# Kernel optimization log

Measured on AMD Instinct MI355X. Metric: run time of the kernel, lower is better.

## Reference

```python
import jax, jax.numpy as jnp
import numpy as np
import math

NUM_HEADS = 16
D_KV = 64
D_MODEL = 1024
NUM_BUCKETS = 32
MAX_DISTANCE = 128
SEQ = 2048
BATCH = 2


def _relative_position_bucket(relative_position):
    # bidirectional T5 bucketing
    num_buckets = NUM_BUCKETS // 2  # 16
    buckets = (relative_position > 0).astype(jnp.int32) * num_buckets
    rp = jnp.abs(relative_position)
    max_exact = num_buckets // 2  # 8
    is_small = rp < max_exact
    rp_safe = jnp.maximum(rp, 1)  # avoid log(0); masked by is_small anyway
    rp_large = max_exact + (
        jnp.log(rp_safe.astype(jnp.float32) / max_exact)
        / math.log(MAX_DISTANCE / max_exact)
        * (num_buckets - max_exact)
    ).astype(jnp.int32)
    rp_large = jnp.minimum(rp_large, num_buckets - 1)
    return buckets + jnp.where(is_small, rp, rp_large)


def _position_bias(rel_bias_table, q_len, k_len):
    ctx = jnp.arange(q_len)[:, None]
    mem = jnp.arange(k_len)[None, :]
    buckets = _relative_position_bucket(mem - ctx)  # (q,k)
    vals = rel_bias_table[buckets]  # (q,k,h)
    return jnp.transpose(vals, (2, 0, 1))[None]  # (1,h,q,k)


def setup_inputs() -> dict:
    key = jax.random.key(0)
    ks = jax.random.split(key, 6)
    s = 1.0 / math.sqrt(D_MODEL)
    return {
        "hidden_states": jax.random.normal(ks[0], (BATCH, SEQ, D_MODEL), jnp.float32),
        "Wq": jax.random.normal(ks[1], (D_MODEL, NUM_HEADS * D_KV), jnp.float32) * s,
        "Wk": jax.random.normal(ks[2], (D_MODEL, NUM_HEADS * D_KV), jnp.float32) * s,
        "Wv": jax.random.normal(ks[3], (D_MODEL, NUM_HEADS * D_KV), jnp.float32) * s,
        "Wo": jax.random.normal(ks[4], (NUM_HEADS * D_KV, D_MODEL), jnp.float32) * s,
        "rel_bias_table": jax.random.normal(ks[5], (NUM_BUCKETS, NUM_HEADS), jnp.float32),
    }


def reference(hidden_states, Wq, Wk, Wv, Wo, rel_bias_table):
    b, s, _ = hidden_states.shape
    q = (hidden_states @ Wq).reshape(b, s, NUM_HEADS, D_KV).transpose(0, 2, 1, 3)
    k = (hidden_states @ Wk).reshape(b, s, NUM_HEADS, D_KV).transpose(0, 2, 1, 3)
    v = (hidden_states @ Wv).reshape(b, s, NUM_HEADS, D_KV).transpose(0, 2, 1, 3)
    # T5: NO query scaling, additive relative-position bias
    scores = jnp.einsum("bhqd,bhkd->bhqk", q, k) + _position_bias(rel_bias_table, s, s)
    attn = jax.nn.softmax(scores, axis=-1)  # dropout is identity in eval
    out = jnp.einsum("bhqk,bhkd->bhqd", attn, v)
    out = out.transpose(0, 2, 1, 3).reshape(b, s, NUM_HEADS * D_KV)
    return out @ Wo
```

## Files before the change

### kernel.cpp

```cpp
#include <hip/hip_runtime.h>
#include <hip/hip_bf16.h>
#include <math.h>

#define NUM_HEADS 16
#define D_KV 64
#define D_MODEL 1024
#define SEQ 2048
#define BATCH 2
#define LOG2E 1.4426950408889634f

using bf16x8 = __attribute__((ext_vector_type(8))) short;
using bf16x4 = __attribute__((ext_vector_type(4))) short;
using f32x4  = __attribute__((ext_vector_type(4))) float;

__device__ inline unsigned short f2bf(float f) {
  union { float f; unsigned int i; } v; v.f = f;
  unsigned int u = v.i;
  return (unsigned short)((u + 0x7FFFu + ((u >> 16) & 1u)) >> 16);
}
__device__ inline unsigned short f2bf_fast(float f) {
  union { float f; unsigned int i; } v; v.f = f;
  return (unsigned short)((v.i + 0x8000u) >> 16);
}

#if __has_builtin(__builtin_amdgcn_exp2f)
#define EXP2(x) __builtin_amdgcn_exp2f(x)
#else
#define EXP2(x) __expf((x) * 0.6931471805599453f)
#endif

__device__ inline unsigned int pk_bf16(float a, float b) {
#if __has_builtin(__builtin_amdgcn_cvt_pk_bf16_f32)
  auto v = __builtin_amdgcn_cvt_pk_bf16_f32(a, b);
  unsigned int u; __builtin_memcpy(&u, &v, 4);
  return u;
#else
  return ((unsigned int)f2bf_fast(b) << 16) | f2bf_fast(a);
#endif
}

__device__ inline void gld_lds16(const unsigned short* g, unsigned short* l) {
  __builtin_amdgcn_global_load_lds(
      (const __attribute__((address_space(1))) unsigned int*)g,
      (__attribute__((address_space(3))) unsigned int*)l, 16, 0, 0);
}

__global__ __launch_bounds__(256) void prep_kernel(const float* __restrict__ X,
                                                   const float* __restrict__ W0,
                                                   const float* __restrict__ W1,
                                                   const float* __restrict__ W2,
                                                   const float* __restrict__ W3,
                                                   const float* __restrict__ tbl,
                                                   unsigned short* __restrict__ xbf,
                                                   unsigned short* __restrict__ wt,
                                                   float* __restrict__ biasF) {
  __shared__ __align__(16) unsigned short T[64][72];
  int bid = blockIdx.x;
  int t = threadIdx.x;
  if (bid < 2048) {
    int i = (bid * 256 + t) * 8;
    __align__(16) unsigned short tmp[8];
#pragma unroll
    for (int e = 0; e < 8; e++) tmp[e] = f2bf(X[i + e]);
    *(uint4*)&xbf[i] = *(uint4*)tmp;
  } else if (bid < 3072) {
    int rem = bid - 2048;
    int z = rem >> 8, tid = rem & 255;
    const float* in = (z == 0) ? W0 : (z == 1) ? W1 : (z == 2) ? W2 : W3;
    unsigned short* o = wt + (long)z * 1048576;
    int r0 = (tid & 15) * 64, c0 = (tid >> 4) * 64;
#pragma unroll
    for (int i = 0; i < 2; i++) {
      int c = t + 256 * i; int r = c >> 3, k8 = (c & 7) * 8;
      const float* src = &in[(long)(r0 + r) * 1024 + c0 + k8];
      __align__(16) unsigned short tmp[8];
#pragma unroll
      for (int e = 0; e < 8; e++) tmp[e] = f2bf(src[e]);
      *(uint4*)&T[r][k8] = *(uint4*)tmp;
    }
    __syncthreads();
#pragma unroll
    for (int i = 0; i < 2; i++) {
      int c = t + 256 * i; int r = c >> 3, k8 = (c & 7) * 8;
      __align__(16) unsigned short tmp[8];
#pragma unroll
      for (int e = 0; e < 8; e++) tmp[e] = T[k8 + e][r];
      *(uint4*)&o[(long)(c0 + r) * 1024 + r0 + k8] = *(uint4*)tmp;
    }
  } else {
#pragma unroll
    for (int ii = 0; ii < 16; ii++) {
      int idx = t + 256 * ii;
      if (idx >= 4095) break;
      int rel = idx - 2047;
      int bucket = (rel > 0) ? 16 : 0;
      int rp = rel < 0 ? -rel : rel;
      int add;
      if (rp < 8) add = rp;
      else {
        int rl = 8 + (int)(logf((float)rp * 0.125f) / logf(16.0f) * 8.0f);
        add = rl < 15 ? rl : 15;
      }
      bucket += add;
#pragma unroll
      for (int h = 0; h < 16; h++) biasF[h * 4096 + idx] = tbl[bucket * 16 + h] * LOG2E;
    }
  }
}

__global__ __launch_bounds__(256) void transpose_b2b(const unsigned short* __restrict__ in,
                                                     unsigned short* __restrict__ out,
                                                     int in_stride, int out_stride,
                                                     long in_bstride, long out_bstride) {
  __shared__ __align__(16) unsigned short T[64][72];
  in  += blockIdx.z * in_bstride;
  out += blockIdx.z * out_bstride;
  int r0 = blockIdx.x * 64, c0 = blockIdx.y * 64;
  int t = threadIdx.x;
#pragma unroll
  for (int i = 0; i < 2; i++) {
    int c = t + 256 * i; int r = c >> 3, k8 = (c & 7) * 8;
    *(uint4*)&T[r][k8] = *(const uint4*)&in[(long)(r0 + r) * in_stride + c0 + k8];
  }
  __syncthreads();
#pragma unroll
  for (int i = 0; i < 2; i++) {
    int c = t + 256 * i; int r = c >> 3, k8 = (c & 7) * 8;
    __align__(16) unsigned short tmp[8];
#pragma unroll
    for (int e = 0; e < 8; e++) tmp[e] = T[k8 + e][r];
    *(uint4*)&out[(long)(c0 + r) * out_stride + r0 + k8] = *(uint4*)tmp;
  }
}

__global__ __launch_bounds__(256) void gemm_kernel(const unsigned short* __restrict__ X,
                                                   const unsigned short* __restrict__ Wt,
                                                   unsigned short* __restrict__ out_b,
                                                   float* __restrict__ out_f, int mode) {
  __shared__ __align__(16) unsigned short As[128 * 32];
  __shared__ __align__(16) unsigned short Bs[128 * 32];
  const int K = 1024;
  int m0 = blockIdx.x * 128;
  int n0 = blockIdx.y * 128;
  const unsigned short* W = Wt + (long)blockIdx.z * 1048576;
  unsigned short* outq = (mode == 0) ? out_b + (long)blockIdx.z * 4194304 : nullptr;
  float scale = (mode == 0 && blockIdx.z == 0) ? LOG2E : 1.0f;
  int t = threadIdx.x;
  int w = t >> 6, l = t & 63;
  int wr = (w >> 1) * 64, wc = (w & 1) * 64;
  int lr = l & 15, lq = l >> 4;
  f32x4 acc[4][4];
#pragma unroll
  for (int i = 0; i < 4; i++)
#pragma unroll
    for (int j = 0; j < 4; j++) acc[i][j] = (f32x4){0.f, 0.f, 0.f, 0.f};

  for (int k0 = 0; k0 < K; k0 += 32) {
#pragma unroll
    for (int i = 0; i < 2; i++) {
      int c = t + 256 * i;
      int r = c >> 2, kc = (c & 3) * 8;
      gld_lds16(&X[(long)(m0 + r) * K + k0 + kc], &As[c * 8]);
      gld_lds16(&W[(long)(n0 + r) * K + k0 + kc], &Bs[c * 8]);
    }
    __syncthreads();
    bf16x8 a[4], b[4];
#pragma unroll
    for (int mi = 0; mi < 4; mi++) a[mi] = *(const bf16x8*)&As[(wr + mi * 16 + lr) * 32 + lq * 8];
#pragma unroll
    for (int ni = 0; ni < 4; ni++) b[ni] = *(const bf16x8*)&Bs[(wc + ni * 16 + lr) * 32 + lq * 8];
#pragma unroll
    for (int mi = 0; mi < 4; mi++)
#pragma unroll
      for (int ni = 0; ni < 4; ni++)
        acc[mi][ni] = __builtin_amdgcn_mfma_f32_16x16x32_bf16(a[mi], b[ni], acc[mi][ni], 0, 0, 0);
    __syncthreads();
  }
#pragma unroll
  for (int mi = 0; mi < 4; mi++)
#pragma unroll
    for (int ni = 0; ni < 4; ni++)
#pragma unroll
      for (int r = 0; r < 4; r++) {
        int m = m0 + wr + mi * 16 + lq * 4 + r;
        int n = n0 + wc + ni * 16 + lr;
        float vf = acc[mi][ni][r] * scale;
        if (mode == 0) {
          int b_ = m >> 11, s = m & 2047, h = n >> 6, d = n & 63;
          outq[(((long)(b_ * NUM_HEADS + h) * SEQ) + s) * 64 + d] = f2bf(vf);
        } else {
          out_f[(long)m * 1024 + n] = vf;
        }
      }
}

__global__ __launch_bounds__(256, 2) void attn_kernel(const unsigned short* __restrict__ Q,
                                                      const unsigned short* __restrict__ Km,
                                                      const unsigned short* __restrict__ Vt,
                                                      const float* __restrict__ biasF,
                                                      unsigned short* __restrict__ O) {
  __shared__ __align__(16) unsigned short Ks[64 * 72];
  __shared__ __align__(16) unsigned short Vs[64 * 72];
  __shared__ __align__(16) float biasRf[2][2176];
  int q0 = blockIdx.x * 128;
  int bh = blockIdx.y;
  int b_ = bh >> 4, h = bh & 15;
  const unsigned short* Qb = Q  + (long)bh * SEQ * 64;
  const unsigned short* Kb = Km + (long)bh * SEQ * 64;
  const unsigned short* Vb = Vt + (long)bh * 64 * SEQ;
  const float* btabF = biasF + h * 4096;
  int t = threadIdx.x;
  int w = t >> 6, l = t & 63;
  int lr = l & 15, lq = l >> 4;
  int qw = w * 32;

  int gbase = 1920 - q0;
  for (int i = t; i < 2176; i += 256) {
    int g0 = gbase + i;     if (g0 > 4094) g0 = 4094;
    int g1 = gbase + i + 1; if (g1 > 4094) g1 = 4094;
    biasRf[0][i] = btabF[g0];
    biasRf[1][i] = btabF[g1];
  }

  bf16x8 aq[2][2];
#pragma unroll
  for (int qt = 0; qt < 2; qt++)
#pragma unroll
    for (int ks = 0; ks < 2; ks++)
      aq[qt][ks] = *(const bf16x8*)&Qb[(long)(q0 + qw + qt * 16 + lr) * 64 + ks * 32 + lq * 8];

  int c0 = t, c1 = t + 256;
  int r0s = c0 >> 3, f0 = (c0 & 7) * 8;
  int r1s = c1 >> 3, f1 = (c1 & 7) * 8;

  uint4 kca = *(const uint4*)&Kb[(long)r0s * 64 + f0];
  uint4 kcb = *(const uint4*)&Kb[(long)r1s * 64 + f1];
  uint4 vca = *(const uint4*)&Vb[(long)r0s * SEQ + f0];
  uint4 vcb = *(const uint4*)&Vb[(long)r1s * SEQ + f1];
  *(uint4*)&Ks[r0s * 72 + f0] = kca;
  *(uint4*)&Ks[r1s * 72 + f1] = kcb;
  *(uint4*)&Vs[r0s * 72 + f0] = vca;
  *(uint4*)&Vs[r1s * 72 + f1] = vcb;

  f32x4 accO[4][2];
  f32x4 accL[2];
#pragma unroll
  for (int qt = 0; qt < 2; qt++) {
    accL[qt] = (f32x4){0.f, 0.f, 0.f, 0.f};
#pragma unroll
    for (int dt = 0; dt < 4; dt++) accO[dt][qt] = (f32x4){0.f, 0.f, 0.f, 0.f};
  }

  bf16x4 ones4;
#pragma unroll
  for (int e = 0; e < 4; e++) ones4[e] = (short)0x3F80;

  int vb = 127 + lq * 4 - qw - lr;
  int bj2 = vb & 1;
  const float* brow = biasRf[bj2];
  int pbc = vb - bj2 - 16;

  for (int k0 = 0; k0 < SEQ; k0 += 64) {
    __syncthreads();
    bool more = (k0 + 64) < SEQ;

    float2 bbl[5][2];
    int pb = pbc + k0;
#pragma unroll
    for (int m = 0; m < 5; m++) {
      bbl[m][0] = *(const float2*)&brow[pb + 16 * m];
      bbl[m][1] = *(const float2*)&brow[pb + 16 * m + 2];
    }

    bf16x8 bk[4][2];
#pragma unroll
    for (int kt = 0; kt < 4; kt++)
#pragma unroll
      for (int ks = 0; ks < 2; ks++)
        bk[kt][ks] = *(const bf16x8*)&Ks[(kt * 16 + lr) * 72 + ks * 32 + lq * 8];

    if (more) {
      const unsigned short* Kn = Kb + (long)(k0 + 64) * 64;
      const unsigned short* Vn = Vb + (k0 + 64);
      kca = *(const uint4*)&Kn[(long)r0s * 64 + f0];
      kcb = *(const uint4*)&Kn[(long)r1s * 64 + f1];
      vca = *(const uint4*)&Vn[(long)r0s * SEQ + f0];
      vcb = *(const uint4*)&Vn[(long)r1s * SEQ + f1];
    }

    f32x4 sacc[4][2];
#pragma unroll
    for (int kt = 0; kt < 4; kt++)
#pragma unroll
      for (int qt = 0; qt < 2; qt++) sacc[kt][qt] = (f32x4){0.f, 0.f, 0.f, 0.f};
#pragma unroll
    for (int ks = 0; ks < 2; ks++)
#pragma unroll
      for (int kt = 0; kt < 4; kt++)
#pragma unroll
        for (int qt = 0; qt < 2; qt++)
          sacc[kt][qt] = __builtin_amdgcn_mfma_f32_16x16x32_bf16(bk[kt][ks], aq[qt][ks], sacc[kt][qt], 0, 0, 0);

    bf16x4 pk[4][2];
#pragma unroll
    for (int kt = 0; kt < 4; kt++)
#pragma unroll
      for (int qt = 0; qt < 2; qt++) {
        int blk = kt - qt + 1;
        float p0 = EXP2(sacc[kt][qt][0] + bbl[blk][0].x);
        float p1 = EXP2(sacc[kt][qt][1] + bbl[blk][0].y);
        float p2 = EXP2(sacc[kt][qt][2] + bbl[blk][1].x);
        float p3 = EXP2(sacc[kt][qt][3] + bbl[blk][1].y);
        unsigned int uu[2] = { pk_bf16(p0, p1), pk_bf16(p2, p3) };
        bf16x4 pv; __builtin_memcpy(&pv, uu, 8);
        pk[kt][qt] = pv;
      }

#pragma unroll
    for (int kt = 0; kt < 4; kt++) {
      bf16x4 va[4];
#pragma unroll
      for (int dt = 0; dt < 4; dt++)
        va[dt] = *(const bf16x4*)&Vs[(dt * 16 + lr) * 72 + kt * 16 + lq * 4];
#pragma unroll
      for (int qt = 0; qt < 2; qt++) {
#pragma unroll
        for (int dt = 0; dt < 4; dt++)
          accO[dt][qt] = __builtin_amdgcn_mfma_f32_16x16x16bf16_1k(va[dt], pk[kt][qt], accO[dt][qt], 0, 0, 0);
        accL[qt] = __builtin_amdgcn_mfma_f32_16x16x16bf16_1k(ones4, pk[kt][qt], accL[qt], 0, 0, 0);
      }
    }

    __syncthreads();
    if (more) {
      *(uint4*)&Ks[r0s * 72 + f0] = kca;
      *(uint4*)&Ks[r1s * 72 + f1] = kcb;
      *(uint4*)&Vs[r0s * 72 + f0] = vca;
      *(uint4*)&Vs[r1s * 72 + f1] = vcb;
    }
  }

#pragma unroll
  for (int qt = 0; qt < 2; qt++) {
    float rl = 1.0f / accL[qt][0];
    int q = q0 + qw + qt * 16 + lr;
#pragma unroll
    for (int dt = 0; dt < 4; dt++) {
      unsigned int s0 = ((unsigned int)f2bf(accO[dt][qt][1] * rl) << 16) | f2bf(accO[dt][qt][0] * rl);
      unsigned int s1 = ((unsigned int)f2bf(accO[dt][qt][3] * rl) << 16) | f2bf(accO[dt][qt][2] * rl);
      *(uint2*)&O[((long)(b_ * SEQ + q)) * 1024 + h * 64 + dt * 16 + lq * 4] = (uint2){s0, s1};
    }
  }
}

extern "C" void kernel_launch(void* const* d_in, const int* in_sizes, int n_in,
                              void* d_out, int out_size, void* d_ws, size_t ws_size,
                              hipStream_t stream) {
  const float* X   = (const float*)d_in[0];
  const float* Wq  = (const float*)d_in[1];
  const float* Wk  = (const float*)d_in[2];
  const float* Wv  = (const float*)d_in[3];
  const float* Wo  = (const float*)d_in[4];
  const float* tbl = (const float*)d_in[5];

  unsigned short* wt    = (unsigned short*)d_ws;
  unsigned short* xbf   = wt + 4 * 1048576;
  unsigned short* q_ws  = xbf + 4194304;
  unsigned short* k_ws  = q_ws + 4194304;
  unsigned short* v_ws  = k_ws + 4194304;
  unsigned short* vt_ws = v_ws + 4194304;
  unsigned short* o_ws  = vt_ws + 4194304;
  float* biasF = (float*)(o_ws + 4194304);

  prep_kernel<<<3073, 256, 0, stream>>>(X, Wq, Wk, Wv, Wo, tbl, xbf, wt, biasF);
  gemm_kernel<<<dim3(32, 8, 3), 256, 0, stream>>>(xbf, wt, q_ws, nullptr, 0);
  transpose_b2b<<<dim3(32, 1, 32), 256, 0, stream>>>(v_ws, vt_ws, 64, 2048, 131072L, 131072L);
  attn_kernel<<<dim3(16, 32), 256, 0, stream>>>(q_ws, k_ws, vt_ws, biasF, o_ws);
  gemm_kernel<<<dim3(32, 8, 1), 256, 0, stream>>>(o_ws, wt + 3 * 1048576, nullptr, (float*)d_out, 1);
}
```

Measured before the change: 216.1 us.

## Fuse V transpose into QKV GEMM epilogue and split attention KV across wave groups

The QKV GEMM now writes V directly in transposed layout, which removes the separate transpose kernel launch and its extra global round trip. The attention kernel moves to 512 threads. Two wave groups each process alternate 64-key blocks for the same 128 queries, and their partial O and row-sum accumulators are merged through shared memory at the end. This doubles the waves available per query tile to hide latency. In exchange it adds a reduction step, uses more LDS, and drops the double bias-row buffer in favour of scalar bias loads.

```diff
diff --git a/kernel.cpp b/kernel.cpp
--- a/kernel.cpp
+++ b/kernel.cpp
@@ -108,34 +108,10 @@
   }
 }
 
-__global__ __launch_bounds__(256) void transpose_b2b(const unsigned short* __restrict__ in,
-                                                     unsigned short* __restrict__ out,
-                                                     int in_stride, int out_stride,
-                                                     long in_bstride, long out_bstride) {
-  __shared__ __align__(16) unsigned short T[64][72];
-  in  += blockIdx.z * in_bstride;
-  out += blockIdx.z * out_bstride;
-  int r0 = blockIdx.x * 64, c0 = blockIdx.y * 64;
-  int t = threadIdx.x;
-#pragma unroll
-  for (int i = 0; i < 2; i++) {
-    int c = t + 256 * i; int r = c >> 3, k8 = (c & 7) * 8;
-    *(uint4*)&T[r][k8] = *(const uint4*)&in[(long)(r0 + r) * in_stride + c0 + k8];
-  }
-  __syncthreads();
-#pragma unroll
-  for (int i = 0; i < 2; i++) {
-    int c = t + 256 * i; int r = c >> 3, k8 = (c & 7) * 8;
-    __align__(16) unsigned short tmp[8];
-#pragma unroll
-    for (int e = 0; e < 8; e++) tmp[e] = T[k8 + e][r];
-    *(uint4*)&out[(long)(c0 + r) * out_stride + r0 + k8] = *(uint4*)tmp;
-  }
-}
-
 __global__ __launch_bounds__(256) void gemm_kernel(const unsigned short* __restrict__ X,
                                                    const unsigned short* __restrict__ Wt,
                                                    unsigned short* __restrict__ out_b,
+                                                   unsigned short* __restrict__ out_vt,
                                                    float* __restrict__ out_f, int mode) {
   __shared__ __align__(16) unsigned short As[128 * 32];
   __shared__ __align__(16) unsigned short Bs[128 * 32];
@@ -176,32 +152,47 @@
         acc[mi][ni] = __builtin_amdgcn_mfma_f32_16x16x32_bf16(a[mi], b[ni], acc[mi][ni], 0, 0, 0);
     __syncthreads();
   }
-#pragma unroll
-  for (int mi = 0; mi < 4; mi++)
-#pragma unroll
-    for (int ni = 0; ni < 4; ni++)
-#pragma unroll
-      for (int r = 0; r < 4; r++) {
-        int m = m0 + wr + mi * 16 + lq * 4 + r;
+
+  if (mode == 0 && blockIdx.z == 2) {
+#pragma unroll
+    for (int mi = 0; mi < 4; mi++)
+#pragma unroll
+      for (int ni = 0; ni < 4; ni++) {
         int n = n0 + wc + ni * 16 + lr;
-        float vf = acc[mi][ni][r] * scale;
-        if (mode == 0) {
-          int b_ = m >> 11, s = m & 2047, h = n >> 6, d = n & 63;
-          outq[(((long)(b_ * NUM_HEADS + h) * SEQ) + s) * 64 + d] = f2bf(vf);
-        } else {
-          out_f[(long)m * 1024 + n] = vf;
+        int h = n >> 6, d = n & 63;
+        int mbase = m0 + wr + mi * 16 + lq * 4;
+        int b2 = mbase >> 11, s = mbase & 2047;
+        unsigned int s0 = ((unsigned int)f2bf(acc[mi][ni][1]) << 16) | f2bf(acc[mi][ni][0]);
+        unsigned int s1 = ((unsigned int)f2bf(acc[mi][ni][3]) << 16) | f2bf(acc[mi][ni][2]);
+        *(uint2*)&out_vt[(((long)(b2 * 16 + h) * 64 + d) << 11) + s] = (uint2){s0, s1};
+      }
+  } else {
+#pragma unroll
+    for (int mi = 0; mi < 4; mi++)
+#pragma unroll
+      for (int ni = 0; ni < 4; ni++)
+#pragma unroll
+        for (int r = 0; r < 4; r++) {
+          int m = m0 + wr + mi * 16 + lq * 4 + r;
+          int n = n0 + wc + ni * 16 + lr;
+          float vf = acc[mi][ni][r] * scale;
+          if (mode == 0) {
+            int b2 = m >> 11, s = m & 2047, h = n >> 6, d = n & 63;
+            outq[(((long)(b2 * NUM_HEADS + h) * SEQ) + s) * 64 + d] = f2bf(vf);
+          } else {
+            out_f[(long)m * 1024 + n] = vf;
+          }
         }
-      }
-}
-
-__global__ __launch_bounds__(256, 2) void attn_kernel(const unsigned short* __restrict__ Q,
-                                                      const unsigned short* __restrict__ Km,
-                                                      const unsigned short* __restrict__ Vt,
-                                                      const float* __restrict__ biasF,
-                                                      unsigned short* __restrict__ O) {
-  __shared__ __align__(16) unsigned short Ks[64 * 72];
-  __shared__ __align__(16) unsigned short Vs[64 * 72];
-  __shared__ __align__(16) float biasRf[2][2176];
+  }
+}
+
+__global__ __launch_bounds__(512) void attn_kernel(const unsigned short* __restrict__ Q,
+                                                   const unsigned short* __restrict__ Km,
+                                                   const unsigned short* __restrict__ Vt,
+                                                   const float* __restrict__ biasF,
+                                                   unsigned short* __restrict__ O) {
+  __shared__ __align__(16) unsigned short KV[4][4608];
+  __shared__ float biasS[2176];
   int q0 = blockIdx.x * 128;
   int bh = blockIdx.y;
   int b_ = bh >> 4, h = bh & 15;
@@ -211,15 +202,14 @@
   const float* btabF = biasF + h * 4096;
   int t = threadIdx.x;
   int w = t >> 6, l = t & 63;
+  int g = w >> 2, wg = w & 3;
   int lr = l & 15, lq = l >> 4;
-  int qw = w * 32;
+  int qw = wg * 32;
 
   int gbase = 1920 - q0;
-  for (int i = t; i < 2176; i += 256) {
-    int g0 = gbase + i;     if (g0 > 4094) g0 = 4094;
-    int g1 = gbase + i + 1; if (g1 > 4094) g1 = 4094;
-    biasRf[0][i] = btabF[g0];
-    biasRf[1][i] = btabF[g1];
+  for (int i = t; i < 2176; i += 512) {
+    int gi = gbase + i; if (gi > 4094) gi = 4094;
+    biasS[i] = btabF[gi];
   }
 
   bf16x8 aq[2][2];
@@ -229,18 +219,16 @@
     for (int ks = 0; ks < 2; ks++)
       aq[qt][ks] = *(const bf16x8*)&Qb[(long)(q0 + qw + qt * 16 + lr) * 64 + ks * 32 + lq * 8];
 
-  int c0 = t, c1 = t + 256;
-  int r0s = c0 >> 3, f0 = (c0 & 7) * 8;
-  int r1s = c1 >> 3, f1 = (c1 & 7) * 8;
-
-  uint4 kca = *(const uint4*)&Kb[(long)r0s * 64 + f0];
-  uint4 kcb = *(const uint4*)&Kb[(long)r1s * 64 + f1];
-  uint4 vca = *(const uint4*)&Vb[(long)r0s * SEQ + f0];
-  uint4 vcb = *(const uint4*)&Vb[(long)r1s * SEQ + f1];
-  *(uint4*)&Ks[r0s * 72 + f0] = kca;
-  *(uint4*)&Ks[r1s * 72 + f1] = kcb;
-  *(uint4*)&Vs[r0s * 72 + f0] = vca;
-  *(uint4*)&Vs[r1s * 72 + f1] = vcb;
+  int rs = t >> 3, fs = (t & 7) * 8;
+
+  uint4 kpa = *(const uint4*)&Kb[(long)rs * 64 + fs];
+  uint4 kpb = *(const uint4*)&Kb[(long)(64 + rs) * 64 + fs];
+  uint4 vpa = *(const uint4*)&Vb[(long)rs * SEQ + fs];
+  uint4 vpb = *(const uint4*)&Vb[(long)rs * SEQ + 64 + fs];
+  *(uint4*)&KV[0][rs * 72 + fs] = kpa;
+  *(uint4*)&KV[1][rs * 72 + fs] = kpb;
+  *(uint4*)&KV[2][rs * 72 + fs] = vpa;
+  *(uint4*)&KV[3][rs * 72 + fs] = vpb;
 
   f32x4 accO[4][2];
   f32x4 accL[2];
@@ -256,36 +244,34 @@
   for (int e = 0; e < 4; e++) ones4[e] = (short)0x3F80;
 
   int vb = 127 + lq * 4 - qw - lr;
-  int bj2 = vb & 1;
-  const float* brow = biasRf[bj2];
-  int pbc = vb - bj2 - 16;
-
-  for (int k0 = 0; k0 < SEQ; k0 += 64) {
-    __syncthreads();
-    bool more = (k0 + 64) < SEQ;
-
-    float2 bbl[5][2];
+  int pbc = vb - 16;
+
+  for (int i = 0; i < 16; i++) {
+    __syncthreads();
+    int k0 = (2 * i + g) * 64;
+    bool more = i < 15;
+
+    float bbl[5][4];
     int pb = pbc + k0;
 #pragma unroll
-    for (int m = 0; m < 5; m++) {
-      bbl[m][0] = *(const float2*)&brow[pb + 16 * m];
-      bbl[m][1] = *(const float2*)&brow[pb + 16 * m + 2];
-    }
+    for (int m = 0; m < 5; m++)
+#pragma unroll
+      for (int j = 0; j < 4; j++) bbl[m][j] = biasS[pb + 16 * m + j];
 
     bf16x8 bk[4][2];
 #pragma unroll
     for (int kt = 0; kt < 4; kt++)
 #pragma unroll
       for (int ks = 0; ks < 2; ks++)
-        bk[kt][ks] = *(const bf16x8*)&Ks[(kt * 16 + lr) * 72 + ks * 32 + lq * 8];
+        bk[kt][ks] = *(const bf16x8*)&KV[g][(kt * 16 + lr) * 72 + ks * 32 + lq * 8];
 
     if (more) {
-      const unsigned short* Kn = Kb + (long)(k0 + 64) * 64;
-      const unsigned short* Vn = Vb + (k0 + 64);
-      kca = *(const uint4*)&Kn[(long)r0s * 64 + f0];
-      kcb = *(const uint4*)&Kn[(long)r1s * 64 + f1];
-      vca = *(const uint4*)&Vn[(long)r0s * SEQ + f0];
-      vcb = *(const uint4*)&Vn[(long)r1s * SEQ + f1];
+      const unsigned short* Kn = Kb + (long)(2 * i + 2) * 64 * 64;
+      const unsigned short* Vn = Vb + (2 * i + 2) * 64;
+      kpa = *(const uint4*)&Kn[(long)rs * 64 + fs];
+      kpb = *(const uint4*)&Kn[(long)(64 + rs) * 64 + fs];
+      vpa = *(const uint4*)&Vn[(long)rs * SEQ + fs];
+      vpb = *(const uint4*)&Vn[(long)rs * SEQ + 64 + fs];
     }
 
     f32x4 sacc[4][2];
@@ -307,10 +293,10 @@
 #pragma unroll
       for (int qt = 0; qt < 2; qt++) {
         int blk = kt - qt + 1;
-        float p0 = EXP2(sacc[kt][qt][0] + bbl[blk][0].x);
-        float p1 = EXP2(sacc[kt][qt][1] + bbl[blk][0].y);
-        float p2 = EXP2(sacc[kt][qt][2] + bbl[blk][1].x);
-        float p3 = EXP2(sacc[kt][qt][3] + bbl[blk][1].y);
+        float p0 = EXP2(sacc[kt][qt][0] + bbl[blk][0]);
+        float p1 = EXP2(sacc[kt][qt][1] + bbl[blk][1]);
+        float p2 = EXP2(sacc[kt][qt][2] + bbl[blk][2]);
+        float p3 = EXP2(sacc[kt][qt][3] + bbl[blk][3]);
         unsigned int uu[2] = { pk_bf16(p0, p1), pk_bf16(p2, p3) };
         bf16x4 pv; __builtin_memcpy(&pv, uu, 8);
         pk[kt][qt] = pv;
@@ -321,7 +307,7 @@
       bf16x4 va[4];
 #pragma unroll
       for (int dt = 0; dt < 4; dt++)
-        va[dt] = *(const bf16x4*)&Vs[(dt * 16 + lr) * 72 + kt * 16 + lq * 4];
+        va[dt] = *(const bf16x4*)&KV[2 + g][(dt * 16 + lr) * 72 + kt * 16 + lq * 4];
 #pragma unroll
       for (int qt = 0; qt < 2; qt++) {
 #pragma unroll
@@ -333,22 +319,52 @@
 
     __syncthreads();
     if (more) {
-      *(uint4*)&Ks[r0s * 72 + f0] = kca;
-      *(uint4*)&Ks[r1s * 72 + f1] = kcb;
-      *(uint4*)&Vs[r0s * 72 + f0] = vca;
-      *(uint4*)&Vs[r1s * 72 + f1] = vcb;
-    }
-  }
-
-#pragma unroll
-  for (int qt = 0; qt < 2; qt++) {
-    float rl = 1.0f / accL[qt][0];
-    int q = q0 + qw + qt * 16 + lr;
-#pragma unroll
-    for (int dt = 0; dt < 4; dt++) {
-      unsigned int s0 = ((unsigned int)f2bf(accO[dt][qt][1] * rl) << 16) | f2bf(accO[dt][qt][0] * rl);
-      unsigned int s1 = ((unsigned int)f2bf(accO[dt][qt][3] * rl) << 16) | f2bf(accO[dt][qt][2] * rl);
-      *(uint2*)&O[((long)(b_ * SEQ + q)) * 1024 + h * 64 + dt * 16 + lq * 4] = (uint2){s0, s1};
+      *(uint4*)&KV[0][rs * 72 + fs] = kpa;
+      *(uint4*)&KV[1][rs * 72 + fs] = kpb;
+      *(uint4*)&KV[2][rs * 72 + fs] = vpa;
+      *(uint4*)&KV[3][rs * 72 + fs] = vpb;
+    }
+  }
+
+  float* mrg = (float*)&KV[0][0];
+  int slot = (wg * 64 + l) * 34;
+  if (g == 1) {
+    float2* mp = (float2*)&mrg[slot];
+    int j = 0;
+#pragma unroll
+    for (int dt = 0; dt < 4; dt++)
+#pragma unroll
+      for (int qt = 0; qt < 2; qt++) {
+        mp[j++] = (float2){accO[dt][qt][0], accO[dt][qt][1]};
+        mp[j++] = (float2){accO[dt][qt][2], accO[dt][qt][3]};
+      }
+    mp[16] = (float2){accL[0][0], accL[1][0]};
+  }
+  __syncthreads();
+  if (g == 0) {
+    const float2* mp = (const float2*)&mrg[slot];
+    int j = 0;
+#pragma unroll
+    for (int dt = 0; dt < 4; dt++)
+#pragma unroll
+      for (int qt = 0; qt < 2; qt++) {
+        float2 a = mp[j++], b2 = mp[j++];
+        accO[dt][qt][0] += a.x;  accO[dt][qt][1] += a.y;
+        accO[dt][qt][2] += b2.x; accO[dt][qt][3] += b2.y;
+      }
+    float2 ls = mp[16];
+    float rl0 = 1.0f / (accL[0][0] + ls.x);
+    float rl1 = 1.0f / (accL[1][0] + ls.y);
+#pragma unroll
+    for (int qt = 0; qt < 2; qt++) {
+      float rl = qt ? rl1 : rl0;
+      int q = q0 + qw + qt * 16 + lr;
+#pragma unroll
+      for (int dt = 0; dt < 4; dt++) {
+        unsigned int s0 = ((unsigned int)f2bf(accO[dt][qt][1] * rl) << 16) | f2bf(accO[dt][qt][0] * rl);
+        unsigned int s1 = ((unsigned int)f2bf(accO[dt][qt][3] * rl) << 16) | f2bf(accO[dt][qt][2] * rl);
+        *(uint2*)&O[((long)(b_ * SEQ + q)) * 1024 + h * 64 + dt * 16 + lq * 4] = (uint2){s0, s1};
+      }
     }
   }
 }
@@ -373,8 +389,7 @@
   float* biasF = (float*)(o_ws + 4194304);
 
   prep_kernel<<<3073, 256, 0, stream>>>(X, Wq, Wk, Wv, Wo, tbl, xbf, wt, biasF);
-  gemm_kernel<<<dim3(32, 8, 3), 256, 0, stream>>>(xbf, wt, q_ws, nullptr, 0);
-  transpose_b2b<<<dim3(32, 1, 32), 256, 0, stream>>>(v_ws, vt_ws, 64, 2048, 131072L, 131072L);
-  attn_kernel<<<dim3(16, 32), 256, 0, stream>>>(q_ws, k_ws, vt_ws, biasF, o_ws);
-  gemm_kernel<<<dim3(32, 8, 1), 256, 0, stream>>>(o_ws, wt + 3 * 1048576, nullptr, (float*)d_out, 1);
-}
+  gemm_kernel<<<dim3(32, 8, 3), 256, 0, stream>>>(xbf, wt, q_ws, vt_ws, nullptr, 0);
+  attn_kernel<<<dim3(16, 32), 512, 0, stream>>>(q_ws, k_ws, vt_ws, biasF, o_ws);
+  gemm_kernel<<<dim3(32, 8, 1), 256, 0, stream>>>(o_ws, wt + 3 * 1048576, nullptr, nullptr, (float*)d_out, 1);
+}
```

Result: no change. 219.5 us (+1.6%).
